# Kernel tuning notes

Measured on AMD Instinct MI355X. Metric: run time of the kernel, lower is better.

The kernel has to match this reference:

```python
import jax, jax.numpy as jnp
import numpy as np

B, T, C, H = 2, 2048, 1024, 16
DH = C // H  # 64


def setup_inputs() -> dict:
    key = jax.random.key(0)
    ks = jax.random.split(key, 8)
    scale = 1.0 / np.sqrt(C)
    x = jax.random.normal(ks[0], (B, T, C), dtype=jnp.float32)
    mask = jax.random.randint(ks[1], (B, T), 0, 2, dtype=jnp.int32)
    Wq = jax.random.normal(ks[2], (C, C), dtype=jnp.float32) * scale
    bq = jnp.zeros((C,), dtype=jnp.float32)
    Wk = jax.random.normal(ks[3], (C, C), dtype=jnp.float32) * scale
    bk = jnp.zeros((C,), dtype=jnp.float32)
    Wv = jax.random.normal(ks[4], (C, C), dtype=jnp.float32) * scale
    bv = jnp.zeros((C,), dtype=jnp.float32)
    return {"x": x, "Wq": Wq, "bq": bq, "Wk": Wk, "bk": bk, "Wv": Wv, "bv": bv, "mask": mask}


def reference(x, Wq, bq, Wk, bk, Wv, bv, mask):
    # q/k/v projections: [B,T,C] -> [B,H,T,DH]
    def proj(W, b):
        return (x @ W + b).reshape(B, T, H, DH).transpose(0, 2, 1, 3)

    q = proj(Wq, bq)
    k = proj(Wk, bk)
    v = proj(Wv, bv)

    att = jnp.einsum("bhqd,bhkd->bhqk", q, k) * (1.0 / np.sqrt(DH))

    # outer-product padding mask: square_mask[b,q,k] = mask[b,q]*mask[b,k]
    m = mask.astype(jnp.float32)
    square_mask = m[:, :, None] * m[:, None, :]           # [B,T,T]
    sm = (square_mask != 0)[:, None, :, :]                 # [B,1,T,T]
    att = jnp.where(sm, att, -jnp.inf)

    # rows that are fully masked (query token padded) -> softmax gives NaN
    # in torch; torch then zeros the NaNs. Replicate with a safe softmax.
    row_valid = (mask != 0)[:, None, :, None]              # [B,1,T,1]
    att_safe = jnp.where(row_valid, att, 0.0)
    att = jax.nn.softmax(att_safe, axis=-1)
    att = jnp.where(row_valid, att, 0.0)
    # attn_pdrop = 0.0 -> dropout is identity

    y = jnp.einsum("bhqk,bhkd->bhqd", att, v)              # [B,H,T,DH]
    y = y.transpose(0, 2, 1, 3).reshape(B, T, C)
    return y
```

## Files before the change

### kernel.cpp

```cpp
#include <hip/hip_runtime.h>

#define B_ 2
#define T_ 2048
#define C_ 1024
#define H_ 16
#define DH_ 64

typedef __attribute__((ext_vector_type(8))) _Float16 half8;
typedef __attribute__((ext_vector_type(4))) _Float16 half4;
typedef __attribute__((ext_vector_type(2))) __fp16 fp16x2;
typedef __attribute__((ext_vector_type(4))) float f32x4;

__device__ __forceinline__ unsigned short f2h(float f) {
    union { _Float16 h; unsigned short u; } cv; cv.h = (_Float16)f; return cv.u;
}
__device__ __forceinline__ unsigned pk2(float a, float b) {
    union { fp16x2 h; unsigned u; } cv;
    cv.h = __builtin_amdgcn_cvt_pkrtz(a, b);
    return cv.u;
}

__device__ __forceinline__ void gll16(const void* g, void* l) {
    __builtin_amdgcn_global_load_lds(
        (const __attribute__((address_space(1))) void*)g,
        (__attribute__((address_space(3))) void*)l, 16, 0, 0);
}

__global__ __launch_bounds__(256) void prep_kernel(
    const float* __restrict__ x, unsigned short* __restrict__ xf,
    const int* __restrict__ mask, unsigned short* __restrict__ mb,
    const float* __restrict__ Wq, const float* __restrict__ Wk,
    const float* __restrict__ Wv, unsigned short* __restrict__ wt)
{
    __shared__ float tile[32][33];
    const int tid = threadIdx.x;

    if (blockIdx.x < 2048) {
        const size_t idx8 = ((size_t)blockIdx.x * 256 + tid) * 8;
        float4 v0 = *(const float4*)(x + idx8);
        float4 v1 = *(const float4*)(x + idx8 + 4);
        float f[8] = {v0.x, v0.y, v0.z, v0.w, v1.x, v1.y, v1.z, v1.w};
        unsigned short h[8];
#pragma unroll
        for (int i = 0; i < 8; i++) h[i] = f2h(f[i]);
        *(uint4*)(xf + idx8) = *(const uint4*)h;

        if (blockIdx.x == 0) {
#pragma unroll
            for (int j = 0; j < 16; j++) {
                int i = tid * 16 + j;
                mb[i] = (mask[i] != 0) ? (unsigned short)0x3C00 : (unsigned short)0;
            }
        }
    } else {
        const int idx = blockIdx.x - 2048;
        const int z   = idx >> 10;
        const int rem = idx & 1023;
        const int n0  = (rem & 31) * 32;
        const int k0  = (rem >> 5) * 32;
        const float* __restrict__ W = (z == 0) ? Wq : (z == 1) ? Wk : Wv;
        unsigned short* __restrict__ wtz = wt + (size_t)z * C_ * C_;
        const int tx = tid & 31;
        const int ty = tid >> 5;
#pragma unroll
        for (int j = 0; j < 4; j++)
            tile[ty + j * 8][tx] = W[(size_t)(k0 + ty + j * 8) * C_ + n0 + tx];
        __syncthreads();
#pragma unroll
        for (int j = 0; j < 4; j++)
            wtz[(size_t)(n0 + ty + j * 8) * C_ + k0 + tx] = f2h(tile[tx][ty + j * 8]);
    }
}

__global__ __launch_bounds__(256) void qkv_mfma_kernel(
    const unsigned short* __restrict__ xf, const unsigned short* __restrict__ wt,
    const float* __restrict__ bq, const float* __restrict__ bk,
    const float* __restrict__ bv, const int* __restrict__ maskp,
    unsigned short* __restrict__ qb, unsigned short* __restrict__ kb,
    unsigned short* __restrict__ vt)
{
    __shared__ unsigned short sX[128 * 64];
    __shared__ unsigned short sW[128 * 64];

    const int z = blockIdx.z;
    const float* __restrict__ bias = (z == 0) ? bq : (z == 1) ? bk : bv;
    const unsigned short* __restrict__ wtz = wt + (size_t)z * C_ * C_;

    const int tok0 = blockIdx.x * 128;
    const int col0 = blockIdx.y * 128;
    const int wv    = threadIdx.x >> 6;
    const int lane  = threadIdx.x & 63;
    const int l15   = lane & 15;
    const int quad  = lane >> 4;
    const int l7    = l15 & 7;
    const int wm    = wv >> 1;
    const int wn    = wv & 1;
    const int lrow8 = lane >> 3;
    const int gch   = (lane & 7) ^ lrow8;

    f32x4 acc[4][4];
#pragma unroll
    for (int i = 0; i < 4; i++)
#pragma unroll
        for (int j = 0; j < 4; j++) acc[i][j] = (f32x4){0.f, 0.f, 0.f, 0.f};

    int aoff[4][2], boff[4][2];
#pragma unroll
    for (int i = 0; i < 4; i++)
#pragma unroll
        for (int s = 0; s < 2; s++) {
            aoff[i][s] = (wm * 64 + i * 16 + l15) * 64 + (((s * 4 + quad) ^ l7) * 8);
            boff[i][s] = (wn * 64 + i * 16 + l15) * 64 + (((s * 4 + quad) ^ l7) * 8);
        }

    const unsigned short* Abuf = (z < 2) ? sX : sW;
    const unsigned short* Bbuf = (z < 2) ? sW : sX;

    for (int k0 = 0; k0 < C_; k0 += 64) {
        __syncthreads();
#pragma unroll
        for (int s = 0; s < 8; ++s) {
            int g    = (s << 2) + wv;
            int tsel = g >> 4;
            int r0   = (g & 15) << 3;
            const unsigned short* src = tsel ? wtz : xf;
            unsigned short*       dst = tsel ? sW  : sX;
            int rowg = tsel ? col0 : tok0;
            gll16(src + (size_t)(rowg + r0 + lrow8) * C_ + k0 + gch * 8,
                  dst + r0 * 64);
        }
        __syncthreads();

        half8 af[4][2], bf_[4][2];
#pragma unroll
        for (int i = 0; i < 4; i++)
#pragma unroll
            for (int s = 0; s < 2; s++) {
                af[i][s]  = *(const half8*)&Abuf[aoff[i][s]];
                bf_[i][s] = *(const half8*)&Bbuf[boff[i][s]];
            }
#pragma unroll
        for (int s = 0; s < 2; s++)
#pragma unroll
            for (int j = 0; j < 4; j++)
#pragma unroll
                for (int i = 0; i < 4; i++)
                    acc[i][j] = __builtin_amdgcn_mfma_f32_16x16x32_f16(
                        af[i][s], bf_[j][s], acc[i][j], 0, 0, 0);
    }

    if (z == 0) {
#pragma unroll
        for (int j = 0; j < 4; j++) {
            int col = col0 + wn * 64 + j * 16 + l15;
            int h = col >> 6, d = col & 63;
            float bs = bias[col];
#pragma unroll
            for (int i = 0; i < 4; i++) {
#pragma unroll
                for (int r = 0; r < 4; r++) {
                    int tok = tok0 + wm * 64 + i * 16 + quad * 4 + r;
                    int bidx = tok >> 11, t = tok & (T_ - 1);
                    qb[((size_t)(bidx * H_ + h) * T_ + t) * DH_ + d] =
                        f2h((acc[i][j][r] + bs) * 0.18033688011112042f);
                }
            }
        }
    } else if (z == 1) {
#pragma unroll
        for (int j = 0; j < 4; j++) {
            int col = col0 + wn * 64 + j * 16 + l15;
            int h = col >> 6, d = col & 63;
            float bs = bias[col];
#pragma unroll
            for (int i = 0; i < 4; i++) {
#pragma unroll
                for (int r = 0; r < 4; r++) {
                    int tok = tok0 + wm * 64 + i * 16 + quad * 4 + r;
                    int bidx = tok >> 11, t = tok & (T_ - 1);
                    kb[((size_t)(bidx * H_ + h) * T_ + t) * DH_ + d] =
                        f2h(acc[i][j][r] + bs);
                }
            }
        }
    } else {
        float mv4[4]; int bidx4[4], t4[4];
#pragma unroll
        for (int j = 0; j < 4; j++) {
            int tok = tok0 + wn * 64 + j * 16 + l15;
            bidx4[j] = tok >> 11; t4[j] = tok & (T_ - 1);
            mv4[j] = (maskp[bidx4[j] * T_ + t4[j]] != 0) ? 1.f : 0.f;
        }
#pragma unroll
        for (int i = 0; i < 4; i++) {
#pragma unroll
            for (int r = 0; r < 4; r++) {
                int col = col0 + wm * 64 + i * 16 + quad * 4 + r;
                int h = col >> 6, d = col & 63;
                float bs = bias[col];
#pragma unroll
                for (int j = 0; j < 4; j++) {
                    vt[((size_t)(bidx4[j] * H_ + h) * DH_ + d) * T_ + t4[j]] =
                        f2h((acc[i][j][r] + bs) * mv4[j]);
                }
            }
        }
    }
}

__global__ __launch_bounds__(256) void attn_mfma_kernel(
    const unsigned short* __restrict__ qb,
    const unsigned short* __restrict__ kb,
    const unsigned short* __restrict__ vt,
    const int* __restrict__ mask,
    const unsigned short* __restrict__ mb,
    float* __restrict__ out)
{
    __shared__ unsigned short Ks[2][64 * 64];
    __shared__ unsigned short Vs[2][64 * 64];

    const int bh   = blockIdx.x;
    const int b    = bh >> 4;
    const int h    = bh & 15;
    const int wv   = threadIdx.x >> 6;
    const int lane = threadIdx.x & 63;
    const int l15  = lane & 15;
    const int quad = lane >> 4;
    const int l7   = l15 & 7;
    const int q0w  = blockIdx.y * 128 + wv * 32;

    const unsigned short* kbh = kb + (size_t)bh * T_ * DH_;
    const unsigned short* vbh = vt + (size_t)bh * DH_ * T_;
    const unsigned short* mbb = mb + b * T_;
    const int* __restrict__ mrow = mask + b * T_;

    half8 qf[2][2];
#pragma unroll
    for (int qt = 0; qt < 2; ++qt)
#pragma unroll
        for (int c = 0; c < 2; ++c)
            qf[qt][c] = *(const half8*)(qb + ((size_t)bh * T_ + q0w + qt * 16 + l15) * DH_
                                        + c * 32 + quad * 8);

    f32x4 o[2][4];
#pragma unroll
    for (int qt = 0; qt < 2; ++qt)
#pragma unroll
        for (int n = 0; n < 4; ++n) o[qt][n] = (f32x4){0.f, 0.f, 0.f, 0.f};
    f32x4 lacc[2];
    lacc[0] = (f32x4){0.f, 0.f, 0.f, 0.f};
    lacc[1] = (f32x4){0.f, 0.f, 0.f, 0.f};

    const int lrow = lane >> 3;
    const int gch  = (lane & 7) ^ lrow;

#pragma unroll
    for (int s = 0; s < 4; ++s) {
        int j  = (wv << 2) + s;
        int rb = j & 7;
        if (j < 8) gll16(kbh + (size_t)(rb * 8 + lrow) * DH_ + gch * 8, &Ks[0][rb * 512]);
        else       gll16(vbh + (size_t)(rb * 8 + lrow) * T_  + gch * 8, &Vs[0][rb * 512]);
    }

    for (int kt = 0; kt < 32; ++kt) {
        const int cur   = kt & 1;
        const int kbase = kt * 64;
        __syncthreads();

        if (kt < 31) {
            const int nb = kbase + 64;
#pragma unroll
            for (int s = 0; s < 4; ++s) {
                int j  = (wv << 2) + s;
                int rb = j & 7;
                if (j < 8) gll16(kbh + (size_t)(nb + rb * 8 + lrow) * DH_ + gch * 8,
                                 &Ks[cur ^ 1][rb * 512]);
                else       gll16(vbh + (size_t)(rb * 8 + lrow) * T_ + nb + gch * 8,
                                 &Vs[cur ^ 1][rb * 512]);
            }
        }

        const unsigned short* Kc = &Ks[cur][0];
        const unsigned short* Vc = &Vs[cur][0];

        half8 kf[4][2];
#pragma unroll
        for (int ktile = 0; ktile < 4; ++ktile)
#pragma unroll
            for (int c = 0; c < 2; ++c)
                kf[ktile][c] = *(const half8*)(Kc + (ktile * 16 + l15) * 64
                                               + (((c * 4 + quad) ^ l7) * 8));

        half4 vb[4][4];
#pragma unroll
        for (int n = 0; n < 4; ++n)
#pragma unroll
            for (int ktile = 0; ktile < 4; ++ktile)
                vb[n][ktile] = *(const half4*)(Vc + (n * 16 + l15) * 64
                                               + (((ktile * 2 + (quad >> 1)) ^ l7) * 8)
                                               + (quad & 1) * 4);

        half4 bmf[4];
#pragma unroll
        for (int ktile = 0; ktile < 4; ++ktile) {
            half4 mv = *(const half4*)(mbb + kbase + ktile * 16 + quad * 4);
            bmf[ktile] = (l15 == 0) ? mv : (half4)0;
        }

#pragma unroll
        for (int qt = 0; qt < 2; ++qt) {
            half4 pa[4];
#pragma unroll
            for (int ktile = 0; ktile < 4; ++ktile) {
                f32x4 st = (f32x4){0.f, 0.f, 0.f, 0.f};
                st = __builtin_amdgcn_mfma_f32_16x16x32_f16(kf[ktile][0], qf[qt][0], st, 0, 0, 0);
                st = __builtin_amdgcn_mfma_f32_16x16x32_f16(kf[ktile][1], qf[qt][1], st, 0, 0, 0);
                union { uint2 u; half4 h; } cv;
                cv.u.x = pk2(__builtin_amdgcn_exp2f(st[0]), __builtin_amdgcn_exp2f(st[1]));
                cv.u.y = pk2(__builtin_amdgcn_exp2f(st[2]), __builtin_amdgcn_exp2f(st[3]));
                pa[ktile] = cv.h;
            }

#pragma unroll
            for (int ktile = 0; ktile < 4; ++ktile)
                lacc[qt] = __builtin_amdgcn_mfma_f32_16x16x16f16(
                    pa[ktile], bmf[ktile], lacc[qt], 0, 0, 0);

#pragma unroll
            for (int n = 0; n < 4; ++n)
#pragma unroll
                for (int ktile = 0; ktile < 4; ++ktile)
                    o[qt][n] = __builtin_amdgcn_mfma_f32_16x16x16f16(
                        pa[ktile], vb[n][ktile], o[qt][n], 0, 0, 0);
        }
    }

#pragma unroll
    for (int qt = 0; qt < 2; ++qt) {
#pragma unroll
        for (int r = 0; r < 4; ++r) {
            float lv = __shfl(lacc[qt][r], quad << 4, 64);
            int q = q0w + qt * 16 + quad * 4 + r;
            float iv = (mrow[q] != 0 && lv > 0.f) ? (1.0f / lv) : 0.f;
            float* orow = out + ((size_t)(b * T_ + q)) * C_ + h * DH_;
#pragma unroll
            for (int n = 0; n < 4; ++n)
                orow[n * 16 + l15] = o[qt][n][r] * iv;
        }
    }
}

extern "C" void kernel_launch(void* const* d_in, const int* in_sizes, int n_in,
                              void* d_out, int out_size, void* d_ws, size_t ws_size,
                              hipStream_t stream)
{
    (void)in_sizes; (void)n_in; (void)out_size; (void)ws_size;
    const float* x  = (const float*)d_in[0];
    const float* Wq = (const float*)d_in[1];
    const float* bq = (const float*)d_in[2];
    const float* Wk = (const float*)d_in[3];
    const float* bk = (const float*)d_in[4];
    const float* Wv = (const float*)d_in[5];
    const float* bv = (const float*)d_in[6];
    const int* mask = (const int*)d_in[7];
    float* out = (float*)d_out;

    const size_t NX = (size_t)B_ * T_ * C_;
    unsigned short* xf = (unsigned short*)d_ws;
    unsigned short* wt = xf + NX;
    unsigned short* qb = wt + (size_t)3 * C_ * C_;
    unsigned short* kb = qb + NX;
    unsigned short* vt = kb + NX;
    unsigned short* mb = vt + NX;

    prep_kernel<<<5120, 256, 0, stream>>>(x, xf, mask, mb, Wq, Wk, Wv, wt);
    qkv_mfma_kernel<<<dim3(32, 8, 3), 256, 0, stream>>>(
        xf, wt, bq, bk, bv, mask, qb, kb, vt);
    attn_mfma_kernel<<<dim3(32, 16), 256, 0, stream>>>(qb, kb, vt, mask, mb, out);
}
```

Before: 168.2 us.

## Store K and V in MFMA fragment-packed layout for direct per-lane loads

The QKV projection now writes K and V into a layout pre-packed to match the MFMA operand fragments of each 64-key tile. The attention kernel can then copy contiguous 512-element chunks into LDS and read them with plain lane*8 offsets, dropping the XOR swizzle and the strided half4 V reads. The cost is scattered global stores in the projection kernel and a layout tied to the attention kernel's fragment mapping.

```diff
diff --git a/kernel.cpp b/kernel.cpp
--- a/kernel.cpp
+++ b/kernel.cpp
@@ -24,6 +24,20 @@
     __builtin_amdgcn_global_load_lds(
         (const __attribute__((address_space(1))) void*)g,
         (__attribute__((address_space(3))) void*)l, 16, 0, 0);
+}
+
+__device__ __forceinline__ size_t kpack(int bh, int key, int dh) {
+    int kt = key >> 6, ktile = (key >> 4) & 3, kl = key & 15;
+    int half = dh >> 5, qd = (dh >> 3) & 3, e = dh & 7;
+    return ((size_t)((bh * 32 + kt) * 8 + ktile * 2 + half) * 512)
+         + (qd * 16 + kl) * 8 + e;
+}
+__device__ __forceinline__ size_t vpack(int bh, int key, int dh) {
+    int kt = key >> 6, ktile = (key >> 4) & 3;
+    int qd = (key >> 2) & 3, j = key & 3;
+    int n = dh >> 4, l15 = dh & 15;
+    return ((size_t)((bh * 32 + kt) * 8 + n * 2 + (ktile >> 1)) * 512)
+         + (qd * 16 + l15) * 8 + (ktile & 1) * 4 + j;
 }
 
 __global__ __launch_bounds__(256) void prep_kernel(
@@ -76,8 +90,8 @@
     const unsigned short* __restrict__ xf, const unsigned short* __restrict__ wt,
     const float* __restrict__ bq, const float* __restrict__ bk,
     const float* __restrict__ bv, const int* __restrict__ maskp,
-    unsigned short* __restrict__ qb, unsigned short* __restrict__ kb,
-    unsigned short* __restrict__ vt)
+    unsigned short* __restrict__ qb, unsigned short* __restrict__ kfr,
+    unsigned short* __restrict__ vfr)
 {
     __shared__ unsigned short sX[128 * 64];
     __shared__ unsigned short sW[128 * 64];
@@ -178,8 +192,7 @@
                 for (int r = 0; r < 4; r++) {
                     int tok = tok0 + wm * 64 + i * 16 + quad * 4 + r;
                     int bidx = tok >> 11, t = tok & (T_ - 1);
-                    kb[((size_t)(bidx * H_ + h) * T_ + t) * DH_ + d] =
-                        f2h(acc[i][j][r] + bs);
+                    kfr[kpack(bidx * H_ + h, t, d)] = f2h(acc[i][j][r] + bs);
                 }
             }
         }
@@ -200,7 +213,7 @@
                 float bs = bias[col];
 #pragma unroll
                 for (int j = 0; j < 4; j++) {
-                    vt[((size_t)(bidx4[j] * H_ + h) * DH_ + d) * T_ + t4[j]] =
+                    vfr[vpack(bidx4[j] * H_ + h, t4[j], d)] =
                         f2h((acc[i][j][r] + bs) * mv4[j]);
                 }
             }
@@ -210,14 +223,14 @@
 
 __global__ __launch_bounds__(256) void attn_mfma_kernel(
     const unsigned short* __restrict__ qb,
-    const unsigned short* __restrict__ kb,
-    const unsigned short* __restrict__ vt,
+    const unsigned short* __restrict__ kfr,
+    const unsigned short* __restrict__ vfr,
     const int* __restrict__ mask,
     const unsigned short* __restrict__ mb,
     float* __restrict__ out)
 {
-    __shared__ unsigned short Ks[2][64 * 64];
-    __shared__ unsigned short Vs[2][64 * 64];
+    __shared__ unsigned short Ks[2][8 * 512];
+    __shared__ unsigned short Vs[2][8 * 512];
 
     const int bh   = blockIdx.x;
     const int b    = bh >> 4;
@@ -226,11 +239,10 @@
     const int lane = threadIdx.x & 63;
     const int l15  = lane & 15;
     const int quad = lane >> 4;
-    const int l7   = l15 & 7;
     const int q0w  = blockIdx.y * 128 + wv * 32;
 
-    const unsigned short* kbh = kb + (size_t)bh * T_ * DH_;
-    const unsigned short* vbh = vt + (size_t)bh * DH_ * T_;
+    const unsigned short* kfp = kfr + (size_t)bh * 131072;
+    const unsigned short* vfp = vfr + (size_t)bh * 131072;
     const unsigned short* mbb = mb + b * T_;
     const int* __restrict__ mrow = mask + b * T_;
 
@@ -251,15 +263,11 @@
     lacc[0] = (f32x4){0.f, 0.f, 0.f, 0.f};
     lacc[1] = (f32x4){0.f, 0.f, 0.f, 0.f};
 
-    const int lrow = lane >> 3;
-    const int gch  = (lane & 7) ^ lrow;
-
 #pragma unroll
     for (int s = 0; s < 4; ++s) {
-        int j  = (wv << 2) + s;
-        int rb = j & 7;
-        if (j < 8) gll16(kbh + (size_t)(rb * 8 + lrow) * DH_ + gch * 8, &Ks[0][rb * 512]);
-        else       gll16(vbh + (size_t)(rb * 8 + lrow) * T_  + gch * 8, &Vs[0][rb * 512]);
+        int c = (wv << 2) + s;
+        if (c < 8) gll16(kfp + (size_t)c * 512 + lane * 8, &Ks[0][c * 512]);
+        else       gll16(vfp + (size_t)(c - 8) * 512 + lane * 8, &Vs[0][(c - 8) * 512]);
     }
 
     for (int kt = 0; kt < 32; ++kt) {
@@ -268,15 +276,14 @@
         __syncthreads();
 
         if (kt < 31) {
-            const int nb = kbase + 64;
+            const size_t nb = (size_t)(kt + 1) * 4096;
 #pragma unroll
             for (int s = 0; s < 4; ++s) {
-                int j  = (wv << 2) + s;
-                int rb = j & 7;
-                if (j < 8) gll16(kbh + (size_t)(nb + rb * 8 + lrow) * DH_ + gch * 8,
-                                 &Ks[cur ^ 1][rb * 512]);
-                else       gll16(vbh + (size_t)(rb * 8 + lrow) * T_ + nb + gch * 8,
-                                 &Vs[cur ^ 1][rb * 512]);
+                int c = (wv << 2) + s;
+                if (c < 8) gll16(kfp + nb + (size_t)c * 512 + lane * 8,
+                                 &Ks[cur ^ 1][c * 512]);
+                else       gll16(vfp + nb + (size_t)(c - 8) * 512 + lane * 8,
+                                 &Vs[cur ^ 1][(c - 8) * 512]);
             }
         }
 
@@ -285,20 +292,13 @@
 
         half8 kf[4][2];
 #pragma unroll
-        for (int ktile = 0; ktile < 4; ++ktile)
-#pragma unroll
-            for (int c = 0; c < 2; ++c)
-                kf[ktile][c] = *(const half8*)(Kc + (ktile * 16 + l15) * 64
-                                               + (((c * 4 + quad) ^ l7) * 8));
-
-        half4 vb[4][4];
-#pragma unroll
-        for (int n = 0; n < 4; ++n)
-#pragma unroll
-            for (int ktile = 0; ktile < 4; ++ktile)
-                vb[n][ktile] = *(const half4*)(Vc + (n * 16 + l15) * 64
-                                               + (((ktile * 2 + (quad >> 1)) ^ l7) * 8)
-                                               + (quad & 1) * 4);
+        for (int c = 0; c < 8; ++c)
+            kf[c >> 1][c & 1] = *(const half8*)(Kc + c * 512 + lane * 8);
+
+        half8 vv[4][2];
+#pragma unroll
+        for (int c = 0; c < 8; ++c)
+            vv[c >> 1][c & 1] = *(const half8*)(Vc + c * 512 + lane * 8);
 
         half4 bmf[4];
 #pragma unroll
@@ -327,11 +327,17 @@
                     pa[ktile], bmf[ktile], lacc[qt], 0, 0, 0);
 
 #pragma unroll
-            for (int n = 0; n < 4; ++n)
-#pragma unroll
-                for (int ktile = 0; ktile < 4; ++ktile)
+            for (int n = 0; n < 4; ++n) {
+#pragma unroll
+                for (int t = 0; t < 2; ++t) {
+                    half4 vlo = __builtin_shufflevector(vv[n][t], vv[n][t], 0, 1, 2, 3);
+                    half4 vhi = __builtin_shufflevector(vv[n][t], vv[n][t], 4, 5, 6, 7);
                     o[qt][n] = __builtin_amdgcn_mfma_f32_16x16x16f16(
-                        pa[ktile], vb[n][ktile], o[qt][n], 0, 0, 0);
+                        pa[t * 2], vlo, o[qt][n], 0, 0, 0);
+                    o[qt][n] = __builtin_amdgcn_mfma_f32_16x16x16f16(
+                        pa[t * 2 + 1], vhi, o[qt][n], 0, 0, 0);
+                }
+            }
         }
     }
 
@@ -366,15 +372,15 @@
     float* out = (float*)d_out;
 
     const size_t NX = (size_t)B_ * T_ * C_;
-    unsigned short* xf = (unsigned short*)d_ws;
-    unsigned short* wt = xf + NX;
-    unsigned short* qb = wt + (size_t)3 * C_ * C_;
-    unsigned short* kb = qb + NX;
-    unsigned short* vt = kb + NX;
-    unsigned short* mb = vt + NX;
+    unsigned short* xf  = (unsigned short*)d_ws;
+    unsigned short* wt  = xf + NX;
+    unsigned short* qb  = wt + (size_t)3 * C_ * C_;
+    unsigned short* kfr = qb + NX;
+    unsigned short* vfr = kfr + NX;
+    unsigned short* mb  = vfr + NX;
 
     prep_kernel<<<5120, 256, 0, stream>>>(x, xf, mask, mb, Wq, Wk, Wv, wt);
     qkv_mfma_kernel<<<dim3(32, 8, 3), 256, 0, stream>>>(
-        xf, wt, bq, bk, bv, mask, qb, kb, vt);
-    attn_mfma_kernel<<<dim3(32, 16), 256, 0, stream>>>(qb, kb, vt, mask, mb, out);
-}
+        xf, wt, bq, bk, bv, mask, qb, kfr, vfr);
+    attn_mfma_kernel<<<dim3(32, 16), 256, 0, stream>>>(qb, kfr, vfr, mask, mb, out);
+}
```

New measurement: 182.6 us. +8.6%, slower.

## Fuse Q and K projections in one block to share the X tile

Applied to the files above, without the earlier changes.

Blocks with z==0 now compute both the Q and K projections, loading each X tile into shared memory once and reusing it against two weight tiles. The V projection stays separate in z==1, and the grid shrinks from three z-slices to two. This cuts repeated global-to-LDS traffic for X, but the QK blocks double their accumulator registers and add LDS, which may lower occupancy and create an imbalanced grid where QK blocks do twice the work of V blocks.

```diff
diff --git a/kernel.cpp b/kernel.cpp
--- a/kernel.cpp
+++ b/kernel.cpp
@@ -79,12 +79,11 @@
     unsigned short* __restrict__ qb, unsigned short* __restrict__ kb,
     unsigned short* __restrict__ vt)
 {
-    __shared__ unsigned short sX[128 * 64];
-    __shared__ unsigned short sW[128 * 64];
+    __shared__ unsigned short sX [128 * 64];
+    __shared__ unsigned short sW0[128 * 64];
+    __shared__ unsigned short sW1[128 * 64];
 
     const int z = blockIdx.z;
-    const float* __restrict__ bias = (z == 0) ? bq : (z == 1) ? bk : bv;
-    const unsigned short* __restrict__ wtz = wt + (size_t)z * C_ * C_;
 
     const int tok0 = blockIdx.x * 128;
     const int col0 = blockIdx.y * 128;
@@ -98,12 +97,6 @@
     const int lrow8 = lane >> 3;
     const int gch   = (lane & 7) ^ lrow8;
 
-    f32x4 acc[4][4];
-#pragma unroll
-    for (int i = 0; i < 4; i++)
-#pragma unroll
-        for (int j = 0; j < 4; j++) acc[i][j] = (f32x4){0.f, 0.f, 0.f, 0.f};
-
     int aoff[4][2], boff[4][2];
 #pragma unroll
     for (int i = 0; i < 4; i++)
@@ -113,77 +106,117 @@
             boff[i][s] = (wn * 64 + i * 16 + l15) * 64 + (((s * 4 + quad) ^ l7) * 8);
         }
 
-    const unsigned short* Abuf = (z < 2) ? sX : sW;
-    const unsigned short* Bbuf = (z < 2) ? sW : sX;
-
-    for (int k0 = 0; k0 < C_; k0 += 64) {
-        __syncthreads();
-#pragma unroll
-        for (int s = 0; s < 8; ++s) {
-            int g    = (s << 2) + wv;
-            int tsel = g >> 4;
-            int r0   = (g & 15) << 3;
-            const unsigned short* src = tsel ? wtz : xf;
-            unsigned short*       dst = tsel ? sW  : sX;
-            int rowg = tsel ? col0 : tok0;
-            gll16(src + (size_t)(rowg + r0 + lrow8) * C_ + k0 + gch * 8,
-                  dst + r0 * 64);
-        }
-        __syncthreads();
-
-        half8 af[4][2], bf_[4][2];
+    if (z == 0) {
+        const unsigned short* wq = wt;
+        const unsigned short* wk = wt + (size_t)C_ * C_;
+
+        f32x4 accq[4][4], acck[4][4];
 #pragma unroll
         for (int i = 0; i < 4; i++)
 #pragma unroll
-            for (int s = 0; s < 2; s++) {
-                af[i][s]  = *(const half8*)&Abuf[aoff[i][s]];
-                bf_[i][s] = *(const half8*)&Bbuf[boff[i][s]];
-            }
-#pragma unroll
-        for (int s = 0; s < 2; s++)
-#pragma unroll
-            for (int j = 0; j < 4; j++)
-#pragma unroll
-                for (int i = 0; i < 4; i++)
-                    acc[i][j] = __builtin_amdgcn_mfma_f32_16x16x32_f16(
-                        af[i][s], bf_[j][s], acc[i][j], 0, 0, 0);
-    }
-
-    if (z == 0) {
+            for (int j = 0; j < 4; j++) {
+                accq[i][j] = (f32x4){0.f, 0.f, 0.f, 0.f};
+                acck[i][j] = (f32x4){0.f, 0.f, 0.f, 0.f};
+            }
+
+        for (int k0 = 0; k0 < C_; k0 += 64) {
+            __syncthreads();
+#pragma unroll
+            for (int s = 0; s < 12; ++s) {
+                int g = (s << 2) + wv;
+                const unsigned short* src;
+                unsigned short* dst;
+                int rowg, r0;
+                if (g < 16)      { src = xf; dst = sX;  rowg = tok0; r0 = g << 3; }
+                else if (g < 32) { src = wq; dst = sW0; rowg = col0; r0 = (g - 16) << 3; }
+                else             { src = wk; dst = sW1; rowg = col0; r0 = (g - 32) << 3; }
+                gll16(src + (size_t)(rowg + r0 + lrow8) * C_ + k0 + gch * 8,
+                      dst + r0 * 64);
+            }
+            __syncthreads();
+
+            half8 af[4][2];
+#pragma unroll
+            for (int i = 0; i < 4; i++)
+#pragma unroll
+                for (int s = 0; s < 2; s++)
+                    af[i][s] = *(const half8*)&sX[aoff[i][s]];
+
+#pragma unroll
+            for (int j = 0; j < 4; j++) {
+                half8 bq0 = *(const half8*)&sW0[boff[j][0]];
+                half8 bq1 = *(const half8*)&sW0[boff[j][1]];
+                half8 bk0 = *(const half8*)&sW1[boff[j][0]];
+                half8 bk1 = *(const half8*)&sW1[boff[j][1]];
+#pragma unroll
+                for (int i = 0; i < 4; i++) {
+                    accq[i][j] = __builtin_amdgcn_mfma_f32_16x16x32_f16(af[i][0], bq0, accq[i][j], 0, 0, 0);
+                    accq[i][j] = __builtin_amdgcn_mfma_f32_16x16x32_f16(af[i][1], bq1, accq[i][j], 0, 0, 0);
+                    acck[i][j] = __builtin_amdgcn_mfma_f32_16x16x32_f16(af[i][0], bk0, acck[i][j], 0, 0, 0);
+                    acck[i][j] = __builtin_amdgcn_mfma_f32_16x16x32_f16(af[i][1], bk1, acck[i][j], 0, 0, 0);
+                }
+            }
+        }
+
 #pragma unroll
         for (int j = 0; j < 4; j++) {
             int col = col0 + wn * 64 + j * 16 + l15;
             int h = col >> 6, d = col & 63;
-            float bs = bias[col];
+            float bsq = bq[col];
+            float bsk = bk[col];
 #pragma unroll
             for (int i = 0; i < 4; i++) {
 #pragma unroll
                 for (int r = 0; r < 4; r++) {
                     int tok = tok0 + wm * 64 + i * 16 + quad * 4 + r;
                     int bidx = tok >> 11, t = tok & (T_ - 1);
-                    qb[((size_t)(bidx * H_ + h) * T_ + t) * DH_ + d] =
-                        f2h((acc[i][j][r] + bs) * 0.18033688011112042f);
+                    size_t base = ((size_t)(bidx * H_ + h) * T_ + t) * DH_ + d;
+                    qb[base] = f2h((accq[i][j][r] + bsq) * 0.18033688011112042f);
+                    kb[base] = f2h(acck[i][j][r] + bsk);
                 }
             }
         }
-    } else if (z == 1) {
-#pragma unroll
-        for (int j = 0; j < 4; j++) {
-            int col = col0 + wn * 64 + j * 16 + l15;
-            int h = col >> 6, d = col & 63;
-            float bs = bias[col];
-#pragma unroll
-            for (int i = 0; i < 4; i++) {
-#pragma unroll
-                for (int r = 0; r < 4; r++) {
-                    int tok = tok0 + wm * 64 + i * 16 + quad * 4 + r;
-                    int bidx = tok >> 11, t = tok & (T_ - 1);
-                    kb[((size_t)(bidx * H_ + h) * T_ + t) * DH_ + d] =
-                        f2h(acc[i][j][r] + bs);
+    } else {
+        const unsigned short* wv_ = wt + (size_t)2 * C_ * C_;
+
+        f32x4 acc[4][4];
+#pragma unroll
+        for (int i = 0; i < 4; i++)
+#pragma unroll
+            for (int j = 0; j < 4; j++) acc[i][j] = (f32x4){0.f, 0.f, 0.f, 0.f};
+
+        for (int k0 = 0; k0 < C_; k0 += 64) {
+            __syncthreads();
+#pragma unroll
+            for (int s = 0; s < 8; ++s) {
+                int g = (s << 2) + wv;
+                const unsigned short* src = (g < 16) ? xf : wv_;
+                unsigned short*       dst = (g < 16) ? sX : sW0;
+                int rowg = (g < 16) ? tok0 : col0;
+                int r0   = (g & 15) << 3;
+                gll16(src + (size_t)(rowg + r0 + lrow8) * C_ + k0 + gch * 8,
+                      dst + r0 * 64);
+            }
+            __syncthreads();
+
+            half8 aw[4][2], bf_[4][2];
+#pragma unroll
+            for (int i = 0; i < 4; i++)
+#pragma unroll
+                for (int s = 0; s < 2; s++) {
+                    aw[i][s]  = *(const half8*)&sW0[aoff[i][s]];
+                    bf_[i][s] = *(const half8*)&sX[boff[i][s]];
                 }
-            }
-        }
-    } else {
+#pragma unroll
+            for (int s = 0; s < 2; s++)
+#pragma unroll
+                for (int j = 0; j < 4; j++)
+#pragma unroll
+                    for (int i = 0; i < 4; i++)
+                        acc[i][j] = __builtin_amdgcn_mfma_f32_16x16x32_f16(
+                            aw[i][s], bf_[j][s], acc[i][j], 0, 0, 0);
+        }
+
         float mv4[4]; int bidx4[4], t4[4];
 #pragma unroll
         for (int j = 0; j < 4; j++) {
@@ -197,7 +230,7 @@
             for (int r = 0; r < 4; r++) {
                 int col = col0 + wm * 64 + i * 16 + quad * 4 + r;
                 int h = col >> 6, d = col & 63;
-                float bs = bias[col];
+                float bs = bv[col];
 #pragma unroll
                 for (int j = 0; j < 4; j++) {
                     vt[((size_t)(bidx4[j] * H_ + h) * DH_ + d) * T_ + t4[j]] =
@@ -374,7 +407,7 @@
     unsigned short* mb = vt + NX;
 
     prep_kernel<<<5120, 256, 0, stream>>>(x, xf, mask, mb, Wq, Wk, Wv, wt);
-    qkv_mfma_kernel<<<dim3(32, 8, 3), 256, 0, stream>>>(
+    qkv_mfma_kernel<<<dim3(32, 8, 2), 256, 0, stream>>>(
         xf, wt, bq, bk, bv, mask, qb, kb, vt);
     attn_mfma_kernel<<<dim3(32, 16), 256, 0, stream>>>(qb, kb, vt, mask, mb, out);
 }
```

Result: slower. 176.2 us (+4.8%).
